# Optimization experiments

Hardware: AMD Instinct MI355X
Metric: run time of the kernel (lower is better)

Reference implementation:

```python
import jax, jax.numpy as jnp
import numpy as np

N = 50000   # nodes
D = 128     # hidden_dim
H = 8       # num_heads
DK = D // H # per-head dim
E = 1600000 # edges
L = 2       # n_layers
LN_EPS = 1e-5


def _layer_norm(x, g, b):
    m = jnp.mean(x, axis=-1, keepdims=True)
    v = jnp.mean(jnp.square(x - m), axis=-1, keepdims=True)
    return (x - m) * jax.lax.rsqrt(v + LN_EPS) * g + b


def _gt_layer(h, src, dst, Wq, bq, Wk, bk, Wv, bv, Wo, bo, W1, b1, W2, b2, g1, be1, g2, be2):
    n = h.shape[0]
    Q = (h @ Wq + bq).reshape(n, H, DK)
    K = (h @ Wk + bk).reshape(n, H, DK)
    V = (h @ Wv + bv).reshape(n, H, DK)
    # per-edge scaled dot-product score: K[src] . Q[dst]
    score = jnp.einsum('ehd,ehd->eh', K[src], Q[dst]) / np.sqrt(DK)
    score = jnp.exp(jnp.clip(score, -5.0, 5.0))            # [E,H]
    wV = jax.ops.segment_sum(V[src] * score[:, :, None], dst, num_segments=n)  # [N,H,DK]
    z = jax.ops.segment_sum(score, dst, num_segments=n)    # [N,H]
    attn = wV / (z[:, :, None] + 1e-6)                     # possible_empty-safe softmax
    h_att = attn.reshape(n, D) @ Wo + bo
    h = _layer_norm(h + h_att, g1, be1)                    # residual + LN
    ffn = jax.nn.relu(h @ W1 + b1) @ W2 + b2
    h = _layer_norm(h + ffn, g2, be2)                      # residual + LN
    return h


def setup_inputs() -> dict:
    key = jax.random.key(0)
    ks = jax.random.split(key, 16)
    s = 1.0 / np.sqrt(D)
    s2 = 1.0 / np.sqrt(2 * D)
    w = lambda k, shape, sc: jax.random.normal(k, shape, jnp.float32) * sc
    return {
        'h':   jax.random.normal(ks[0], (N, D), jnp.float32),
        'src': jax.random.randint(ks[1], (E,), 0, N),
        'dst': jax.random.randint(ks[2], (E,), 0, N),
        'Wq': w(ks[3], (L, D, D), s), 'bq': jnp.zeros((L, D), jnp.float32),
        'Wk': w(ks[4], (L, D, D), s), 'bk': jnp.zeros((L, D), jnp.float32),
        'Wv': w(ks[5], (L, D, D), s), 'bv': jnp.zeros((L, D), jnp.float32),
        'Wo': w(ks[6], (L, D, D), s), 'bo': jnp.zeros((L, D), jnp.float32),
        'W1': w(ks[7], (L, D, 2 * D), s), 'b1': jnp.zeros((L, 2 * D), jnp.float32),
        'W2': w(ks[8], (L, 2 * D, D), s2), 'b2': jnp.zeros((L, D), jnp.float32),
        'ln1_g': jnp.ones((L, D), jnp.float32), 'ln1_b': jnp.zeros((L, D), jnp.float32),
        'ln2_g': jnp.ones((L, D), jnp.float32), 'ln2_b': jnp.zeros((L, D), jnp.float32),
    }


def reference(h, src, dst, Wq, bq, Wk, bk, Wv, bv, Wo, bo, W1, b1, W2, b2, ln1_g, ln1_b, ln2_g, ln2_b):
    for l in range(L):
        h = _gt_layer(h, src, dst, Wq[l], bq[l], Wk[l], bk[l], Wv[l], bv[l],
                      Wo[l], bo[l], W1[l], b1[l], W2[l], b2[l],
                      ln1_g[l], ln1_b[l], ln2_g[l], ln2_b[l])
    return h
```

## Files before the change

### kernel.cpp

```cpp
#include <hip/hip_runtime.h>

#define NN 50000
#define DD 128
#define HH 8
#define EE 1600000
#define LL 2

typedef unsigned short u16;
typedef __attribute__((ext_vector_type(8))) __bf16 bf16x8;
typedef __attribute__((ext_vector_type(4))) float f32x4;
typedef __attribute__((ext_vector_type(2))) float f32x2;

__device__ __forceinline__ float bf2f(u16 u){
    return __uint_as_float(((unsigned int)u) << 16);
}
__device__ __forceinline__ u16 f2bf(float f){
    unsigned int x = __float_as_uint(f);
    x = x + 0x7fff + ((x >> 16) & 1);
    return (u16)(x >> 16);
}

__device__ __forceinline__ void async16(const u16* g, u16* l){
    __builtin_amdgcn_global_load_lds(
        (const __attribute__((address_space(1))) unsigned int*)(const void*)g,
        (__attribute__((address_space(3))) unsigned int*)(void*)l, 16, 0, 0);
}

#define FILL_SUB 128
#define PREP_BLOCKS (1024 + 6250 + 384 + 768)

__global__ __launch_bounds__(256) void prep_kernel(
        const int* __restrict__ dst, int* __restrict__ cnt,
        const float* __restrict__ h_in, u16* __restrict__ hb,
        const float* __restrict__ Wq, const float* __restrict__ Wk, const float* __restrict__ Wv,
        const float* __restrict__ bq, const float* __restrict__ bk, const float* __restrict__ bv,
        u16* __restrict__ WtQKV, float* __restrict__ bQKV,
        const float* __restrict__ Wo, const float* __restrict__ W1, const float* __restrict__ W2,
        u16* __restrict__ WtO, u16* __restrict__ WtF1, u16* __restrict__ WtF2){
    int b = blockIdx.x;
    if (b < 1024){
        int slice = b & 7;
        int sub = b >> 3;
        int lo = slice * (NN / 8), hi = lo + (NN / 8);
        for (int e = sub * 256 + threadIdx.x; e < EE; e += FILL_SUB * 256){
            int d = dst[e];
            if (d >= lo && d < hi) atomicAdd(&cnt[d], 1);
        }
        return;
    }
    b -= 1024;
    if (b < 6250){
        int i = b * 256 + threadIdx.x;
        if (i < NN * DD / 4){
            float4 v = ((const float4*)h_in)[i];
            ushort4 o;
            o.x = f2bf(v.x); o.y = f2bf(v.y); o.z = f2bf(v.z); o.w = f2bf(v.w);
            ((ushort4*)hb)[i] = o;
        }
        return;
    }
    b -= 6250;
    if (b < 384){
        int l = b / 192;
        int idx = (b % 192) * 256 + threadIdx.x;
        if (idx < 384 * 128){
            int n = idx >> 7, k = idx & 127;
            const float* W = (n < 128) ? Wq : (n < 256) ? Wk : Wv;
            int nc = n & 127;
            WtQKV[(size_t)l * 384 * 128 + idx] = f2bf(W[(size_t)l * 128 * 128 + k * 128 + nc]);
            if (k == 0){
                const float* bb = (n < 128) ? bq : (n < 256) ? bk : bv;
                bQKV[l * 384 + n] = bb[l * 128 + nc];
            }
        }
        return;
    }
    b -= 384;
    {
        int which = b / 256;
        int rem = b % 256;
        int l = rem / 128;
        int idx = (rem % 128) * 256 + threadIdx.x;
        const float* in; u16* out; int R, C;
        if (which == 0){ in = Wo; out = WtO; R = 128; C = 128; }
        else if (which == 1){ in = W1; out = WtF1; R = 128; C = 256; }
        else { in = W2; out = WtF2; R = 256; C = 128; }
        int total = R * C;
        if (idx < total){
            size_t mat = (size_t)l * total;
            int r = idx / C, c = idx % C;
            out[mat + (size_t)c * R + r] = f2bf(in[mat + idx]);
        }
    }
}

__global__ __launch_bounds__(1024) void scan_kernel(const int* __restrict__ cnt,
                                                    int* __restrict__ offs, int* __restrict__ cur){
    __shared__ int wsum[16];
    __shared__ int carry_s;
    __shared__ int ctot_s;
    int t = threadIdx.x, lane = t & 63, w = t >> 6;
    if (t == 0){ offs[0] = 0; cur[0] = 0; carry_s = 0; }
    __syncthreads();
    const int N4 = NN / 4;
    for (int base = 0; base < N4; base += 1024){
        int i4 = base + t;
        int4 x = (i4 < N4) ? ((const int4*)cnt)[i4] : make_int4(0, 0, 0, 0);
        int s1 = x.x, s2 = s1 + x.y, s3 = s2 + x.z, s4 = s3 + x.w;
        int v = s4;
        #pragma unroll
        for (int d = 1; d < 64; d <<= 1){ int u = __shfl_up(v, d); if (lane >= d) v += u; }
        if (lane == 63) wsum[w] = v;
        __syncthreads();
        if (t < 16){
            int sv = wsum[t];
            int iv = sv;
            #pragma unroll
            for (int d = 1; d < 16; d <<= 1){ int u = __shfl_up(iv, d); if (t >= d) iv += u; }
            wsum[t] = iv - sv;
            if (t == 15) ctot_s = iv;
        }
        __syncthreads();
        int excl = carry_s + wsum[w] + (v - s4);
        if (i4 < N4){
            int o = 4 * i4;
            offs[o + 1] = excl + s1;  cur[o + 1] = excl + s1;
            offs[o + 2] = excl + s2;  cur[o + 2] = excl + s2;
            offs[o + 3] = excl + s3;  cur[o + 3] = excl + s3;
            offs[o + 4] = excl + s4;  cur[o + 4] = excl + s4;
        }
        __syncthreads();
        if (t == 0) carry_s += ctot_s;
        __syncthreads();
    }
}

__global__ __launch_bounds__(256) void fill_kernel(const int* __restrict__ src, const int* __restrict__ dst,
                                                   int* __restrict__ cur, int* __restrict__ srcs){
    int slice = blockIdx.x & 7;
    int sub = blockIdx.x >> 3;
    int lo = slice * (NN / 8), hi = lo + (NN / 8);
    for (int e = sub * 256 + threadIdx.x; e < EE; e += FILL_SUB * 256){
        int d = dst[e];
        if (d >= lo && d < hi){
            int p = atomicAdd(&cur[d], 1);
            srcs[p] = src[e];
        }
    }
}

#define BM 128
#define LDC 136

__device__ __forceinline__ void stage_tile(const u16* __restrict__ A, const u16* __restrict__ Wt,
                                           u16* As, u16* Bs, int M, int K, int m0, int n0, int k0,
                                           int w, int lane){
    int lr = lane >> 3;
    int swz = ((lane & 7) ^ lr) * 8;
    #pragma unroll
    for (int p = 0; p < 4; p++){
        int s = p * 4 + w;
        int ga = m0 + s * 8 + lr;
        if (ga >= M) ga = M - 1;
        async16(A + (size_t)ga * K + k0 + swz, As + s * 512);
        async16(Wt + (size_t)(n0 + s * 8 + lr) * K + k0 + swz, Bs + s * 512);
    }
}

__device__ __forceinline__ void mfma_tiles(const u16* As, const u16* Bs, f32x4 (&acc)[4][4],
                                           int wm, int wn, int l15, int hi){
    #pragma unroll
    for (int ks = 0; ks < 2; ks++){
        bf16x8 a[4], b[4];
        int ca = ((ks * 4 + hi) ^ (l15 & 7)) * 8;
        #pragma unroll
        for (int i = 0; i < 4; i++){
            a[i] = *(const bf16x8*)(As + (wm * 64 + i * 16 + l15) * 64 + ca);
            b[i] = *(const bf16x8*)(Bs + (wn * 64 + i * 16 + l15) * 64 + ca);
        }
        #pragma unroll
        for (int mi = 0; mi < 4; mi++)
            #pragma unroll
            for (int ni = 0; ni < 4; ni++)
                acc[mi][ni] = __builtin_amdgcn_mfma_f32_16x16x32_bf16(a[mi], b[ni], acc[mi][ni], 0, 0, 0);
    }
}

#define GEMM_LOOP(K)                                                          \
    for (int k0 = 0; k0 < (K); k0 += 64){                                     \
        __syncthreads();                                                      \
        stage_tile(A, Wt, As, Bs, M, (K), m0, n0, k0, w, lane);               \
        asm volatile("s_waitcnt vmcnt(0)" ::: "memory");                      \
        __syncthreads();                                                      \
        mfma_tiles(As, Bs, acc, wm, wn, l15, hi);                             \
    }

__global__ __launch_bounds__(256) void gemm_qkv(const u16* __restrict__ A, const u16* __restrict__ Wt,
                                                const float* __restrict__ bias,
                                                u16* __restrict__ Qb, u16* __restrict__ Kb,
                                                unsigned char* __restrict__ Vb, int M){
    __shared__ __align__(16) char smem[128 * LDC * 2];
    u16* As = (u16*)smem;
    u16* Bs = As + 8192;
    u16* Cs = (u16*)smem;

    int tid = threadIdx.x;
    int m0 = blockIdx.x * BM, n0 = blockIdx.y * 128;
    int lane = tid & 63, w = tid >> 6;
    int wm = w >> 1, wn = w & 1;
    int l15 = lane & 15, hi = lane >> 4;

    f32x4 acc[4][4];
    #pragma unroll
    for (int mi = 0; mi < 4; mi++)
        #pragma unroll
        for (int ni = 0; ni < 4; ni++)
            acc[mi][ni] = (f32x4){0.f, 0.f, 0.f, 0.f};

    GEMM_LOOP(128)

    __syncthreads();
    #pragma unroll
    for (int mi = 0; mi < 4; mi++)
        #pragma unroll
        for (int ni = 0; ni < 4; ni++){
            int col = wn * 64 + ni * 16 + l15;
            float bval = bias[n0 + col];
            #pragma unroll
            for (int j = 0; j < 4; j++){
                int rl = wm * 64 + mi * 16 + hi * 4 + j;
                Cs[rl * LDC + col] = f2bf(acc[mi][ni][j] + bval);
            }
        }
    __syncthreads();
    int qrow = tid >> 4, quad = tid & 15;
    if (n0 < 256){
        u16* Tb = (n0 == 0) ? Qb : Kb;
        #pragma unroll
        for (int p = 0; p < 8; p++){
            int rl = p * 16 + qrow;
            int gr = m0 + rl;
            if (gr < M){
                uint4 v = *(const uint4*)(&Cs[rl * LDC + quad * 8]);
                *(uint4*)(Tb + (size_t)gr * 128 + quad * 8) = v;
            }
        }
    } else {
        #pragma unroll
        for (int p = 0; p < 8; p++){
            int rl = p * 16 + qrow;
            int gr = m0 + rl;
            if (gr < M){
                uint4 v = *(const uint4*)(&Cs[rl * LDC + quad * 8]);
                float f0 = bf2f((u16)(v.x & 0xffff)), f1 = bf2f((u16)(v.x >> 16));
                float f2 = bf2f((u16)(v.y & 0xffff)), f3 = bf2f((u16)(v.y >> 16));
                float f4 = bf2f((u16)(v.z & 0xffff)), f5 = bf2f((u16)(v.z >> 16));
                float f6 = bf2f((u16)(v.w & 0xffff)), f7 = bf2f((u16)(v.w >> 16));
                unsigned int w0 = __builtin_amdgcn_cvt_pk_fp8_f32(f0, f1, 0u, false);
                w0 = __builtin_amdgcn_cvt_pk_fp8_f32(f2, f3, w0, true);
                unsigned int w1 = __builtin_amdgcn_cvt_pk_fp8_f32(f4, f5, 0u, false);
                w1 = __builtin_amdgcn_cvt_pk_fp8_f32(f6, f7, w1, true);
                *(uint2*)(Vb + (size_t)gr * 128 + quad * 8) = make_uint2(w0, w1);
            }
        }
    }
}

__global__ __launch_bounds__(256) void gemm_ln(const u16* __restrict__ A, const u16* __restrict__ Wt,
                                               const float* __restrict__ bias, const u16* __restrict__ resid,
                                               const float* __restrict__ g, const float* __restrict__ b,
                                               u16* __restrict__ out_bf, int M){
    __shared__ __align__(16) u16 As[8192];
    __shared__ __align__(16) u16 Bs[8192];
    __shared__ float ps[2][128];
    __shared__ float pss[2][128];

    int tid = threadIdx.x;
    int m0 = blockIdx.x * BM;
    const int n0 = 0;
    int lane = tid & 63, w = tid >> 6;
    int wm = w >> 1, wn = w & 1;
    int l15 = lane & 15, hi = lane >> 4;

    f32x4 acc[4][4];
    #pragma unroll
    for (int mi = 0; mi < 4; mi++)
        #pragma unroll
        for (int ni = 0; ni < 4; ni++)
            acc[mi][ni] = (f32x4){0.f, 0.f, 0.f, 0.f};

    GEMM_LOOP(128)

    float gcol[4], bcol[4], bval[4];
    #pragma unroll
    for (int ni = 0; ni < 4; ni++){
        int col = wn * 64 + ni * 16 + l15;
        gcol[ni] = g[col]; bcol[ni] = b[col]; bval[ni] = bias[col];
    }

    #pragma unroll
    for (int mi = 0; mi < 4; mi++)
        #pragma unroll
        for (int j = 0; j < 4; j++){
            int rl = wm * 64 + mi * 16 + hi * 4 + j;
            int gr = m0 + rl;
            float s = 0.f, ss = 0.f;
            #pragma unroll
            for (int ni = 0; ni < 4; ni++){
                int col = wn * 64 + ni * 16 + l15;
                float x = acc[mi][ni][j] + bval[ni];
                if (gr < M) x += bf2f(resid[(size_t)gr * 128 + col]);
                acc[mi][ni][j] = x;
                s += x; ss += x * x;
            }
            #pragma unroll
            for (int d = 1; d < 16; d <<= 1){
                s  += __shfl_xor(s, d);
                ss += __shfl_xor(ss, d);
            }
            if (l15 == 0){ ps[wn][rl] = s; pss[wn][rl] = ss; }
        }
    __syncthreads();

    #pragma unroll
    for (int mi = 0; mi < 4; mi++)
        #pragma unroll
        for (int j = 0; j < 4; j++){
            int rl = wm * 64 + mi * 16 + hi * 4 + j;
            int gr = m0 + rl;
            if (gr >= M) continue;
            float s = ps[0][rl] + ps[1][rl];
            float ss = pss[0][rl] + pss[1][rl];
            float mean = s * (1.f / 128.f);
            float var = ss * (1.f / 128.f) - mean * mean;
            float r = rsqrtf(var + 1e-5f);
            #pragma unroll
            for (int ni = 0; ni < 4; ni++){
                int col = wn * 64 + ni * 16 + l15;
                float o = (acc[mi][ni][j] - mean) * r * gcol[ni] + bcol[ni];
                out_bf[(size_t)gr * 128 + col] = f2bf(o);
            }
        }
}

__global__ __launch_bounds__(256) void ffn_ln_kernel(const u16* __restrict__ h1,
                                                     const u16* __restrict__ W1t, const float* __restrict__ b1,
                                                     const u16* __restrict__ W2t, const float* __restrict__ b2,
                                                     const float* __restrict__ g, const float* __restrict__ b,
                                                     u16* __restrict__ out_bf, float* __restrict__ out_f,
                                                     int M){
    __shared__ __align__(16) u16 As[4096];
    __shared__ __align__(16) u16 Bs[16384];
    __shared__ __align__(16) u16 mid[16384];
    __shared__ float ps[2][64];
    __shared__ float pss[2][64];

    int tid = threadIdx.x, lane = tid & 63, w = tid >> 6;
    int l15 = lane & 15, hi = lane >> 4;
    int m0 = blockIdx.x * 64;
    int lr = lane >> 3;
    int swz = ((lane & 7) ^ lr) * 8;

    f32x4 acc1[4][4];
    #pragma unroll
    for (int mi = 0; mi < 4; mi++)
        #pragma unroll
        for (int ni = 0; ni < 4; ni++)
            acc1[mi][ni] = (f32x4){0.f, 0.f, 0.f, 0.f};

    for (int kh = 0; kh < 2; kh++){
        __syncthreads();
        #pragma unroll
        for (int p = 0; p < 2; p++){
            int s = p * 4 + w;
            int ga = m0 + s * 8 + lr;
            if (ga >= M) ga = M - 1;
            async16(h1 + (size_t)ga * 128 + kh * 64 + swz, As + s * 512);
        }
        #pragma unroll
        for (int p = 0; p < 8; p++){
            int s = p * 4 + w;
            int row = s * 8 + lr;
            async16(W1t + (size_t)row * 128 + kh * 64 + swz, Bs + s * 512);
        }
        asm volatile("s_waitcnt vmcnt(0)" ::: "memory");
        __syncthreads();
        #pragma unroll
        for (int ks = 0; ks < 2; ks++){
            int ca = ((ks * 4 + hi) ^ (l15 & 7)) * 8;
            bf16x8 a[4], bb[4];
            #pragma unroll
            for (int i = 0; i < 4; i++){
                a[i] = *(const bf16x8*)(As + (i * 16 + l15) * 64 + ca);
                bb[i] = *(const bf16x8*)(Bs + (w * 64 + i * 16 + l15) * 64 + ca);
            }
            #pragma unroll
            for (int mi = 0; mi < 4; mi++)
                #pragma unroll
                for (int ni = 0; ni < 4; ni++)
                    acc1[mi][ni] = __builtin_amdgcn_mfma_f32_16x16x32_bf16(a[mi], bb[ni], acc1[mi][ni], 0, 0, 0);
        }
    }

    #pragma unroll
    for (int ni = 0; ni < 4; ni++){
        float bv = b1[w * 64 + ni * 16 + l15];
        int kcol = ni * 16 + l15;
        #pragma unroll
        for (int mi = 0; mi < 4; mi++)
            #pragma unroll
            for (int j = 0; j < 4; j++){
                int row = mi * 16 + hi * 4 + j;
                float v = fmaxf(acc1[mi][ni][j] + bv, 0.f);
                mid[w * 4096 + row * 64 + (((kcol >> 3) ^ (row & 7)) * 8 + (kcol & 7))] = f2bf(v);
            }
    }

    int wm = w >> 1, wn = w & 1;
    f32x4 acc2[2][4];
    #pragma unroll
    for (int mi = 0; mi < 2; mi++)
        #pragma unroll
        for (int ni = 0; ni < 4; ni++)
            acc2[mi][ni] = (f32x4){0.f, 0.f, 0.f, 0.f};

    for (int kt = 0; kt < 4; kt++){
        __syncthreads();
        #pragma unroll
        for (int p = 0; p < 4; p++){
            int s = p * 4 + w;
            int row = s * 8 + lr;
            async16(W2t + (size_t)row * 256 + kt * 64 + swz, Bs + s * 512);
        }
        asm volatile("s_waitcnt vmcnt(0)" ::: "memory");
        __syncthreads();
        #pragma unroll
        for (int ks = 0; ks < 2; ks++){
            int ca = ((ks * 4 + hi) ^ (l15 & 7)) * 8;
            bf16x8 a[2], bb[4];
            #pragma unroll
            for (int i = 0; i < 2; i++)
                a[i] = *(const bf16x8*)(mid + kt * 4096 + (wm * 32 + i * 16 + l15) * 64 + ca);
            #pragma unroll
            for (int i = 0; i < 4; i++)
                bb[i] = *(const bf16x8*)(Bs + (wn * 64 + i * 16 + l15) * 64 + ca);
            #pragma unroll
            for (int mi = 0; mi < 2; mi++)
                #pragma unroll
                for (int ni = 0; ni < 4; ni++)
                    acc2[mi][ni] = __builtin_amdgcn_mfma_f32_16x16x32_bf16(a[mi], bb[ni], acc2[mi][ni], 0, 0, 0);
        }
    }

    float gcol[4], bcol[4], bval[4];
    #pragma unroll
    for (int ni = 0; ni < 4; ni++){
        int col = wn * 64 + ni * 16 + l15;
        gcol[ni] = g[col]; bcol[ni] = b[col]; bval[ni] = b2[col];
    }

    #pragma unroll
    for (int mi = 0; mi < 2; mi++)
        #pragma unroll
        for (int j = 0; j < 4; j++){
            int row = wm * 32 + mi * 16 + hi * 4 + j;
            int gr = m0 + row;
            float s = 0.f, ss = 0.f;
            #pragma unroll
            for (int ni = 0; ni < 4; ni++){
                int col = wn * 64 + ni * 16 + l15;
                float x = acc2[mi][ni][j] + bval[ni];
                if (gr < M) x += bf2f(h1[(size_t)gr * 128 + col]);
                acc2[mi][ni][j] = x;
                s += x; ss += x * x;
            }
            #pragma unroll
            for (int d = 1; d < 16; d <<= 1){
                s  += __shfl_xor(s, d);
                ss += __shfl_xor(ss, d);
            }
            if (l15 == 0){ ps[wn][row] = s; pss[wn][row] = ss; }
        }
    __syncthreads();

    #pragma unroll
    for (int mi = 0; mi < 2; mi++)
        #pragma unroll
        for (int j = 0; j < 4; j++){
            int row = wm * 32 + mi * 16 + hi * 4 + j;
            int gr = m0 + row;
            if (gr >= M) continue;
            float s = ps[0][row] + ps[1][row];
            float ss = pss[0][row] + pss[1][row];
            float mean = s * (1.f / 128.f);
            float var = ss * (1.f / 128.f) - mean * mean;
            float r = rsqrtf(var + 1e-5f);
            #pragma unroll
            for (int ni = 0; ni < 4; ni++){
                int col = wn * 64 + ni * 16 + l15;
                float o = (acc2[mi][ni][j] - mean) * r * gcol[ni] + bcol[ni];
                if (out_f) out_f[(size_t)gr * 128 + col] = o;
                else       out_bf[(size_t)gr * 128 + col] = f2bf(o);
            }
        }
}

__global__ __launch_bounds__(256) void edge_attn_kernel(const u16* __restrict__ Qb,
                                                        const u16* __restrict__ Kb,
                                                        const unsigned char* __restrict__ Vb,
                                                        const int* __restrict__ srcs,
                                                        const int* __restrict__ offs,
                                                        u16* __restrict__ att){
    int n = blockIdx.x * 4 + (threadIdx.x >> 6);
    if (n >= NN) return;
    int lane = threadIdx.x & 63;
    int laneh = lane & 31;
    int half = lane >> 5;

    float q0, q1, q2, q3;
    {
        uint2 qv = *(const uint2*)(Qb + (size_t)n * 128 + 4 * laneh);
        q0 = bf2f((u16)(qv.x & 0xffff)); q1 = bf2f((u16)(qv.x >> 16));
        q2 = bf2f((u16)(qv.y & 0xffff)); q3 = bf2f((u16)(qv.y >> 16));
    }
    const u16* kbase = Kb + 4 * laneh;
    const unsigned char* vbase = Vb + 4 * laneh;

    float w0 = 0.f, w1 = 0.f, w2 = 0.f, w3 = 0.f, z = 0.f;
    const float CS = 0.25f * 1.44269504f;

    auto proc = [&](uint2 kk, unsigned int vv, float gate){
        float k0 = bf2f((u16)(kk.x & 0xffff)), k1 = bf2f((u16)(kk.x >> 16));
        float k2 = bf2f((u16)(kk.y & 0xffff)), k3 = bf2f((u16)(kk.y >> 16));
        float p = q0 * k0 + q1 * k1 + q2 * k2 + q3 * k3;
        p += __shfl_xor(p, 1);
        p += __shfl_xor(p, 2);
        p = __builtin_amdgcn_fmed3f(p, -20.f, 20.f);
        float sc = __builtin_amdgcn_exp2f(p * CS) * gate;
        f32x2 vl = __builtin_amdgcn_cvt_pk_f32_fp8(vv, false);
        f32x2 vh = __builtin_amdgcn_cvt_pk_f32_fp8(vv, true);
        w0 += sc * vl[0]; w1 += sc * vl[1]; w2 += sc * vh[0]; w3 += sc * vh[1];
        z += sc;
    };

    int e0 = offs[n], e1 = offs[n + 1];
    int i = e0;
    for (; i + 15 < e1; i += 16){
        int s[8];
        #pragma unroll
        for (int u = 0; u < 8; u++) s[u] = srcs[i + 2 * u + half];
        uint2 kk[8];
        unsigned int vv[8];
        #pragma unroll
        for (int u = 0; u < 8; u++){
            kk[u] = *(const uint2*)(kbase + (size_t)s[u] * 128);
            vv[u] = *(const unsigned int*)(vbase + (size_t)s[u] * 128);
        }
        #pragma unroll
        for (int u = 0; u < 8; u++) proc(kk[u], vv[u], 1.f);
    }
    for (; i + 1 < e1; i += 2){
        int s = srcs[i + half];
        proc(*(const uint2*)(kbase + (size_t)s * 128),
             *(const unsigned int*)(vbase + (size_t)s * 128), 1.f);
    }
    if (i < e1){
        int s = srcs[i];
        proc(*(const uint2*)(kbase + (size_t)s * 128),
             *(const unsigned int*)(vbase + (size_t)s * 128), half ? 0.f : 1.f);
    }

    w0 += __shfl_xor(w0, 32); w1 += __shfl_xor(w1, 32);
    w2 += __shfl_xor(w2, 32); w3 += __shfl_xor(w3, 32);
    z  += __shfl_xor(z, 32);

    if (!half){
        float inv = 1.f / (z + 1e-6f);
        unsigned int oA = (unsigned int)f2bf(w0 * inv) | ((unsigned int)f2bf(w1 * inv) << 16);
        unsigned int oB = (unsigned int)f2bf(w2 * inv) | ((unsigned int)f2bf(w3 * inv) << 16);
        *(uint2*)(att + (size_t)n * DD + 4 * laneh) = make_uint2(oA, oB);
    }
}

extern "C" void kernel_launch(void* const* d_in, const int* in_sizes, int n_in,
                              void* d_out, int out_size, void* d_ws, size_t ws_size,
                              hipStream_t stream){
    const float* h_in = (const float*)d_in[0];
    const int* src  = (const int*)d_in[1];
    const int* dst  = (const int*)d_in[2];
    const float* Wq = (const float*)d_in[3];
    const float* bq = (const float*)d_in[4];
    const float* Wk = (const float*)d_in[5];
    const float* bk = (const float*)d_in[6];
    const float* Wv = (const float*)d_in[7];
    const float* bv = (const float*)d_in[8];
    const float* Wo = (const float*)d_in[9];
    const float* bo = (const float*)d_in[10];
    const float* W1 = (const float*)d_in[11];
    const float* b1 = (const float*)d_in[12];
    const float* W2 = (const float*)d_in[13];
    const float* b2 = (const float*)d_in[14];
    const float* ln1_g = (const float*)d_in[15];
    const float* ln1_b = (const float*)d_in[16];
    const float* ln2_g = (const float*)d_in[17];
    const float* ln2_b = (const float*)d_in[18];
    float* outp = (float*)d_out;

    char* ws = (char*)d_ws;
    auto alloc = [&](size_t bytes) -> char* {
        char* p = ws;
        ws += (bytes + 255) & ~(size_t)255;
        return p;
    };
    int* cnt   = (int*)alloc((size_t)NN * 4);
    int* offs  = (int*)alloc((size_t)(NN + 1) * 4);
    int* cur   = (int*)alloc((size_t)(NN + 1) * 4);
    int* srcs  = (int*)alloc((size_t)EE * 4);
    u16* WtQKV = (u16*)alloc((size_t)LL * 384 * 128 * 2);
    float* bQKV = (float*)alloc((size_t)LL * 384 * 4);
    u16* WtO   = (u16*)alloc((size_t)LL * 128 * 128 * 2);
    u16* WtF1  = (u16*)alloc((size_t)LL * 256 * 128 * 2);
    u16* WtF2  = (u16*)alloc((size_t)LL * 128 * 256 * 2);
    u16* hb    = (u16*)alloc((size_t)NN * DD * 2);
    u16* Qb    = (u16*)alloc((size_t)NN * 128 * 2);
    u16* Kb    = (u16*)alloc((size_t)NN * 128 * 2);
    unsigned char* Vb = (unsigned char*)alloc((size_t)NN * 128);
    u16* att   = (u16*)alloc((size_t)NN * DD * 2);
    u16* h1    = (u16*)alloc((size_t)NN * DD * 2);
    u16* hmid  = (u16*)alloc((size_t)NN * DD * 2);

    hipMemsetAsync(cnt, 0, (size_t)NN * 4, stream);
    prep_kernel<<<PREP_BLOCKS, 256, 0, stream>>>(dst, cnt, h_in, hb,
                                                 Wq, Wk, Wv, bq, bk, bv, WtQKV, bQKV,
                                                 Wo, W1, W2, WtO, WtF1, WtF2);
    scan_kernel<<<1, 1024, 0, stream>>>(cnt, offs, cur);
    fill_kernel<<<8 * FILL_SUB, 256, 0, stream>>>(src, dst, cur, srcs);

    const int MB = (NN + BM - 1) / BM;
    const int MB64 = (NN + 63) / 64;
    const u16* hcur = hb;
    for (int l = 0; l < LL; l++){
        gemm_qkv<<<dim3(MB, 3), 256, 0, stream>>>(hcur, WtQKV + (size_t)l * 384 * 128,
                                                  bQKV + l * 384, Qb, Kb, Vb, NN);
        edge_attn_kernel<<<NN / 4, 256, 0, stream>>>(Qb, Kb, Vb, srcs, offs, att);
        gemm_ln<<<MB, 256, 0, stream>>>(att, WtO + (size_t)l * 128 * 128, bo + l * 128,
                                        hcur, ln1_g + l * 128, ln1_b + l * 128,
                                        h1, NN);
        if (l == LL - 1)
            ffn_ln_kernel<<<MB64, 256, 0, stream>>>(h1, WtF1 + (size_t)l * 256 * 128, b1 + l * 256,
                                                    WtF2 + (size_t)l * 128 * 256, b2 + l * 128,
                                                    ln2_g + l * 128, ln2_b + l * 128,
                                                    nullptr, outp, NN);
        else
            ffn_ln_kernel<<<MB64, 256, 0, stream>>>(h1, WtF1 + (size_t)l * 256 * 128, b1 + l * 256,
                                                    WtF2 + (size_t)l * 128 * 256, b2 + l * 128,
                                                    ln2_g + l * 128, ln2_b + l * 128,
                                                    hmid, nullptr, NN);
        hcur = hmid;
    }
}
```

Baseline: 472.9 us.

## Fuse output projection, first LayerNorm and FFN into one tail kernel

Merges the O-projection GEMM with residual+LayerNorm and the FFN+LayerNorm kernel into a single per-64-row tile kernel. The intermediate h1 stays in shared memory (swizzled) rather than being written to and re-read from global memory, and one kernel launch per layer is removed. In exchange, the W1 computation is split into two N-halves with a smaller Bs buffer, shared memory per block and register pressure change, and the O-projection now uses 64-row tiles instead of BM-row tiles.

```diff
diff --git a/kernel.cpp b/kernel.cpp
--- a/kernel.cpp
+++ b/kernel.cpp
@@ -266,107 +266,35 @@
     }
 }
 
-__global__ __launch_bounds__(256) void gemm_ln(const u16* __restrict__ A, const u16* __restrict__ Wt,
-                                               const float* __restrict__ bias, const u16* __restrict__ resid,
-                                               const float* __restrict__ g, const float* __restrict__ b,
-                                               u16* __restrict__ out_bf, int M){
-    __shared__ __align__(16) u16 As[8192];
+__global__ __launch_bounds__(256) void tail_kernel(const u16* __restrict__ att,
+                                                   const u16* __restrict__ WtO, const float* __restrict__ bo,
+                                                   const u16* __restrict__ resid,
+                                                   const float* __restrict__ g1, const float* __restrict__ b1v,
+                                                   const u16* __restrict__ W1t, const float* __restrict__ b1f,
+                                                   const u16* __restrict__ W2t, const float* __restrict__ b2f,
+                                                   const float* __restrict__ g2, const float* __restrict__ b2v,
+                                                   u16* __restrict__ out_bf, float* __restrict__ out_f,
+                                                   int M){
+    __shared__ __align__(16) u16 h1c[8192];
+    __shared__ __align__(16) u16 mid[16384];
     __shared__ __align__(16) u16 Bs[8192];
-    __shared__ float ps[2][128];
-    __shared__ float pss[2][128];
-
-    int tid = threadIdx.x;
-    int m0 = blockIdx.x * BM;
-    const int n0 = 0;
-    int lane = tid & 63, w = tid >> 6;
-    int wm = w >> 1, wn = w & 1;
-    int l15 = lane & 15, hi = lane >> 4;
-
-    f32x4 acc[4][4];
-    #pragma unroll
-    for (int mi = 0; mi < 4; mi++)
-        #pragma unroll
-        for (int ni = 0; ni < 4; ni++)
-            acc[mi][ni] = (f32x4){0.f, 0.f, 0.f, 0.f};
-
-    GEMM_LOOP(128)
-
-    float gcol[4], bcol[4], bval[4];
-    #pragma unroll
-    for (int ni = 0; ni < 4; ni++){
-        int col = wn * 64 + ni * 16 + l15;
-        gcol[ni] = g[col]; bcol[ni] = b[col]; bval[ni] = bias[col];
-    }
-
-    #pragma unroll
-    for (int mi = 0; mi < 4; mi++)
-        #pragma unroll
-        for (int j = 0; j < 4; j++){
-            int rl = wm * 64 + mi * 16 + hi * 4 + j;
-            int gr = m0 + rl;
-            float s = 0.f, ss = 0.f;
-            #pragma unroll
-            for (int ni = 0; ni < 4; ni++){
-                int col = wn * 64 + ni * 16 + l15;
-                float x = acc[mi][ni][j] + bval[ni];
-                if (gr < M) x += bf2f(resid[(size_t)gr * 128 + col]);
-                acc[mi][ni][j] = x;
-                s += x; ss += x * x;
-            }
-            #pragma unroll
-            for (int d = 1; d < 16; d <<= 1){
-                s  += __shfl_xor(s, d);
-                ss += __shfl_xor(ss, d);
-            }
-            if (l15 == 0){ ps[wn][rl] = s; pss[wn][rl] = ss; }
-        }
-    __syncthreads();
-
-    #pragma unroll
-    for (int mi = 0; mi < 4; mi++)
-        #pragma unroll
-        for (int j = 0; j < 4; j++){
-            int rl = wm * 64 + mi * 16 + hi * 4 + j;
-            int gr = m0 + rl;
-            if (gr >= M) continue;
-            float s = ps[0][rl] + ps[1][rl];
-            float ss = pss[0][rl] + pss[1][rl];
-            float mean = s * (1.f / 128.f);
-            float var = ss * (1.f / 128.f) - mean * mean;
-            float r = rsqrtf(var + 1e-5f);
-            #pragma unroll
-            for (int ni = 0; ni < 4; ni++){
-                int col = wn * 64 + ni * 16 + l15;
-                float o = (acc[mi][ni][j] - mean) * r * gcol[ni] + bcol[ni];
-                out_bf[(size_t)gr * 128 + col] = f2bf(o);
-            }
-        }
-}
-
-__global__ __launch_bounds__(256) void ffn_ln_kernel(const u16* __restrict__ h1,
-                                                     const u16* __restrict__ W1t, const float* __restrict__ b1,
-                                                     const u16* __restrict__ W2t, const float* __restrict__ b2,
-                                                     const float* __restrict__ g, const float* __restrict__ b,
-                                                     u16* __restrict__ out_bf, float* __restrict__ out_f,
-                                                     int M){
-    __shared__ __align__(16) u16 As[4096];
-    __shared__ __align__(16) u16 Bs[16384];
-    __shared__ __align__(16) u16 mid[16384];
     __shared__ float ps[2][64];
     __shared__ float pss[2][64];
+    u16* AsO = mid;
 
     int tid = threadIdx.x, lane = tid & 63, w = tid >> 6;
     int l15 = lane & 15, hi = lane >> 4;
+    int wm = w >> 1, wn = w & 1;
     int m0 = blockIdx.x * 64;
     int lr = lane >> 3;
     int swz = ((lane & 7) ^ lr) * 8;
 
-    f32x4 acc1[4][4];
-    #pragma unroll
-    for (int mi = 0; mi < 4; mi++)
+    f32x4 acc0[2][4];
+    #pragma unroll
+    for (int mi = 0; mi < 2; mi++)
         #pragma unroll
         for (int ni = 0; ni < 4; ni++)
-            acc1[mi][ni] = (f32x4){0.f, 0.f, 0.f, 0.f};
+            acc0[mi][ni] = (f32x4){0.f, 0.f, 0.f, 0.f};
 
     for (int kh = 0; kh < 2; kh++){
         __syncthreads();
@@ -375,48 +303,139 @@
             int s = p * 4 + w;
             int ga = m0 + s * 8 + lr;
             if (ga >= M) ga = M - 1;
-            async16(h1 + (size_t)ga * 128 + kh * 64 + swz, As + s * 512);
-        }
-        #pragma unroll
-        for (int p = 0; p < 8; p++){
+            async16(att + (size_t)ga * 128 + kh * 64 + swz, AsO + s * 512);
+        }
+        #pragma unroll
+        for (int p = 0; p < 4; p++){
             int s = p * 4 + w;
             int row = s * 8 + lr;
-            async16(W1t + (size_t)row * 128 + kh * 64 + swz, Bs + s * 512);
+            async16(WtO + (size_t)row * 128 + kh * 64 + swz, Bs + s * 512);
         }
         asm volatile("s_waitcnt vmcnt(0)" ::: "memory");
         __syncthreads();
         #pragma unroll
         for (int ks = 0; ks < 2; ks++){
             int ca = ((ks * 4 + hi) ^ (l15 & 7)) * 8;
-            bf16x8 a[4], bb[4];
-            #pragma unroll
-            for (int i = 0; i < 4; i++){
-                a[i] = *(const bf16x8*)(As + (i * 16 + l15) * 64 + ca);
-                bb[i] = *(const bf16x8*)(Bs + (w * 64 + i * 16 + l15) * 64 + ca);
-            }
-            #pragma unroll
-            for (int mi = 0; mi < 4; mi++)
+            bf16x8 a[2], bb[4];
+            #pragma unroll
+            for (int i = 0; i < 2; i++)
+                a[i] = *(const bf16x8*)(AsO + (wm * 32 + i * 16 + l15) * 64 + ca);
+            #pragma unroll
+            for (int i = 0; i < 4; i++)
+                bb[i] = *(const bf16x8*)(Bs + (wn * 64 + i * 16 + l15) * 64 + ca);
+            #pragma unroll
+            for (int mi = 0; mi < 2; mi++)
                 #pragma unroll
                 for (int ni = 0; ni < 4; ni++)
-                    acc1[mi][ni] = __builtin_amdgcn_mfma_f32_16x16x32_bf16(a[mi], bb[ni], acc1[mi][ni], 0, 0, 0);
-        }
-    }
-
-    #pragma unroll
-    for (int ni = 0; ni < 4; ni++){
-        float bv = b1[w * 64 + ni * 16 + l15];
-        int kcol = ni * 16 + l15;
-        #pragma unroll
-        for (int mi = 0; mi < 4; mi++)
+                    acc0[mi][ni] = __builtin_amdgcn_mfma_f32_16x16x32_bf16(a[mi], bb[ni], acc0[mi][ni], 0, 0, 0);
+        }
+    }
+
+    {
+        float gc[4], bc[4], bv[4];
+        #pragma unroll
+        for (int ni = 0; ni < 4; ni++){
+            int col = wn * 64 + ni * 16 + l15;
+            gc[ni] = g1[col]; bc[ni] = b1v[col]; bv[ni] = bo[col];
+        }
+        #pragma unroll
+        for (int mi = 0; mi < 2; mi++)
             #pragma unroll
             for (int j = 0; j < 4; j++){
-                int row = mi * 16 + hi * 4 + j;
-                float v = fmaxf(acc1[mi][ni][j] + bv, 0.f);
-                mid[w * 4096 + row * 64 + (((kcol >> 3) ^ (row & 7)) * 8 + (kcol & 7))] = f2bf(v);
-            }
-    }
-
-    int wm = w >> 1, wn = w & 1;
+                int row = wm * 32 + mi * 16 + hi * 4 + j;
+                int gr = m0 + row;
+                float s = 0.f, ss = 0.f;
+                #pragma unroll
+                for (int ni = 0; ni < 4; ni++){
+                    int col = wn * 64 + ni * 16 + l15;
+                    float x = acc0[mi][ni][j] + bv[ni];
+                    if (gr < M) x += bf2f(resid[(size_t)gr * 128 + col]);
+                    acc0[mi][ni][j] = x;
+                    s += x; ss += x * x;
+                }
+                #pragma unroll
+                for (int d = 1; d < 16; d <<= 1){
+                    s  += __shfl_xor(s, d);
+                    ss += __shfl_xor(ss, d);
+                }
+                if (l15 == 0){ ps[wn][row] = s; pss[wn][row] = ss; }
+            }
+        __syncthreads();
+        #pragma unroll
+        for (int mi = 0; mi < 2; mi++)
+            #pragma unroll
+            for (int j = 0; j < 4; j++){
+                int row = wm * 32 + mi * 16 + hi * 4 + j;
+                float s = ps[0][row] + ps[1][row];
+                float ss = pss[0][row] + pss[1][row];
+                float mean = s * (1.f / 128.f);
+                float var = ss * (1.f / 128.f) - mean * mean;
+                float r = rsqrtf(var + 1e-5f);
+                #pragma unroll
+                for (int ni = 0; ni < 4; ni++){
+                    int kcol = ni * 16 + l15;
+                    float o = (acc0[mi][ni][j] - mean) * r * gc[ni] + bc[ni];
+                    h1c[wn * 4096 + row * 64 + (((kcol >> 3) ^ (row & 7)) * 8 + (kcol & 7))] = f2bf(o);
+                }
+            }
+    }
+
+    f32x4 acc1[2][2][4];
+    #pragma unroll
+    for (int nh = 0; nh < 2; nh++)
+        #pragma unroll
+        for (int mi = 0; mi < 2; mi++)
+            #pragma unroll
+            for (int ni = 0; ni < 4; ni++)
+                acc1[nh][mi][ni] = (f32x4){0.f, 0.f, 0.f, 0.f};
+
+    for (int nh = 0; nh < 2; nh++){
+        for (int kh = 0; kh < 2; kh++){
+            __syncthreads();
+            #pragma unroll
+            for (int p = 0; p < 4; p++){
+                int s = p * 4 + w;
+                int row = s * 8 + lr;
+                async16(W1t + (size_t)(nh * 128 + row) * 128 + kh * 64 + swz, Bs + s * 512);
+            }
+            asm volatile("s_waitcnt vmcnt(0)" ::: "memory");
+            __syncthreads();
+            #pragma unroll
+            for (int ks = 0; ks < 2; ks++){
+                int ca = ((ks * 4 + hi) ^ (l15 & 7)) * 8;
+                bf16x8 a[2], bb[4];
+                #pragma unroll
+                for (int i = 0; i < 2; i++)
+                    a[i] = *(const bf16x8*)(h1c + kh * 4096 + (wm * 32 + i * 16 + l15) * 64 + ca);
+                #pragma unroll
+                for (int i = 0; i < 4; i++)
+                    bb[i] = *(const bf16x8*)(Bs + (wn * 64 + i * 16 + l15) * 64 + ca);
+                #pragma unroll
+                for (int mi = 0; mi < 2; mi++)
+                    #pragma unroll
+                    for (int ni = 0; ni < 4; ni++)
+                        acc1[nh][mi][ni] = __builtin_amdgcn_mfma_f32_16x16x32_bf16(a[mi], bb[ni], acc1[nh][mi][ni], 0, 0, 0);
+            }
+        }
+    }
+    __syncthreads();
+    #pragma unroll
+    for (int nh = 0; nh < 2; nh++)
+        #pragma unroll
+        for (int ni = 0; ni < 4; ni++){
+            float bv = b1f[nh * 128 + wn * 64 + ni * 16 + l15];
+            int kcol = ni * 16 + l15;
+            int chunk = nh * 2 + wn;
+            #pragma unroll
+            for (int mi = 0; mi < 2; mi++)
+                #pragma unroll
+                for (int j = 0; j < 4; j++){
+                    int row = wm * 32 + mi * 16 + hi * 4 + j;
+                    float v = fmaxf(acc1[nh][mi][ni][j] + bv, 0.f);
+                    mid[chunk * 4096 + row * 64 + (((kcol >> 3) ^ (row & 7)) * 8 + (kcol & 7))] = f2bf(v);
+                }
+        }
+
     f32x4 acc2[2][4];
     #pragma unroll
     for (int mi = 0; mi < 2; mi++)
@@ -452,25 +471,24 @@
         }
     }
 
-    float gcol[4], bcol[4], bval[4];
+    float gc2[4], bc2[4], bv2[4];
     #pragma unroll
     for (int ni = 0; ni < 4; ni++){
         int col = wn * 64 + ni * 16 + l15;
-        gcol[ni] = g[col]; bcol[ni] = b[col]; bval[ni] = b2[col];
-    }
-
+        gc2[ni] = g2[col]; bc2[ni] = b2v[col]; bv2[ni] = b2f[col];
+    }
+    __syncthreads();
     #pragma unroll
     for (int mi = 0; mi < 2; mi++)
         #pragma unroll
         for (int j = 0; j < 4; j++){
             int row = wm * 32 + mi * 16 + hi * 4 + j;
-            int gr = m0 + row;
             float s = 0.f, ss = 0.f;
             #pragma unroll
             for (int ni = 0; ni < 4; ni++){
-                int col = wn * 64 + ni * 16 + l15;
-                float x = acc2[mi][ni][j] + bval[ni];
-                if (gr < M) x += bf2f(h1[(size_t)gr * 128 + col]);
+                int kcol = ni * 16 + l15;
+                float h1v = bf2f(h1c[wn * 4096 + row * 64 + (((kcol >> 3) ^ (row & 7)) * 8 + (kcol & 7))]);
+                float x = acc2[mi][ni][j] + bv2[ni] + h1v;
                 acc2[mi][ni][j] = x;
                 s += x; ss += x * x;
             }
@@ -498,7 +516,7 @@
             #pragma unroll
             for (int ni = 0; ni < 4; ni++){
                 int col = wn * 64 + ni * 16 + l15;
-                float o = (acc2[mi][ni][j] - mean) * r * gcol[ni] + bcol[ni];
+                float o = (acc2[mi][ni][j] - mean) * r * gc2[ni] + bc2[ni];
                 if (out_f) out_f[(size_t)gr * 128 + col] = o;
                 else       out_bf[(size_t)gr * 128 + col] = f2bf(o);
             }
@@ -626,7 +644,6 @@
     u16* Kb    = (u16*)alloc((size_t)NN * 128 * 2);
     unsigned char* Vb = (unsigned char*)alloc((size_t)NN * 128);
     u16* att   = (u16*)alloc((size_t)NN * DD * 2);
-    u16* h1    = (u16*)alloc((size_t)NN * DD * 2);
     u16* hmid  = (u16*)alloc((size_t)NN * DD * 2);
 
     hipMemsetAsync(cnt, 0, (size_t)NN * 4, stream);
@@ -643,19 +660,20 @@
         gemm_qkv<<<dim3(MB, 3), 256, 0, stream>>>(hcur, WtQKV + (size_t)l * 384 * 128,
                                                   bQKV + l * 384, Qb, Kb, Vb, NN);
         edge_attn_kernel<<<NN / 4, 256, 0, stream>>>(Qb, Kb, Vb, srcs, offs, att);
-        gemm_ln<<<MB, 256, 0, stream>>>(att, WtO + (size_t)l * 128 * 128, bo + l * 128,
-                                        hcur, ln1_g + l * 128, ln1_b + l * 128,
-                                        h1, NN);
         if (l == LL - 1)
-            ffn_ln_kernel<<<MB64, 256, 0, stream>>>(h1, WtF1 + (size_t)l * 256 * 128, b1 + l * 256,
-                                                    WtF2 + (size_t)l * 128 * 256, b2 + l * 128,
-                                                    ln2_g + l * 128, ln2_b + l * 128,
-                                                    nullptr, outp, NN);
+            tail_kernel<<<MB64, 256, 0, stream>>>(att, WtO + (size_t)l * 128 * 128, bo + l * 128,
+                                                  hcur, ln1_g + l * 128, ln1_b + l * 128,
+                                                  WtF1 + (size_t)l * 256 * 128, b1 + l * 256,
+                                                  WtF2 + (size_t)l * 128 * 256, b2 + l * 128,
+                                                  ln2_g + l * 128, ln2_b + l * 128,
+                                                  nullptr, outp, NN);
         else
-            ffn_ln_kernel<<<MB64, 256, 0, stream>>>(h1, WtF1 + (size_t)l * 256 * 128, b1 + l * 256,
-                                                    WtF2 + (size_t)l * 128 * 256, b2 + l * 128,
-                                                    ln2_g + l * 128, ln2_b + l * 128,
-                                                    hmid, nullptr, NN);
+            tail_kernel<<<MB64, 256, 0, stream>>>(att, WtO + (size_t)l * 128 * 128, bo + l * 128,
+                                                  hcur, ln1_g + l * 128, ln1_b + l * 128,
+                                                  WtF1 + (size_t)l * 256 * 128, b1 + l * 256,
+                                                  WtF2 + (size_t)l * 128 * 256, b2 + l * 128,
+                                                  ln2_g + l * 128, ln2_b + l * 128,
+                                                  hmid, nullptr, NN);
         hcur = hmid;
     }
 }
```

New measurement: 455.9 us, median of 2. 1.04x faster.
